# Kernel tuning notes

Measured on AMD Instinct MI355X. Metric: run time of the kernel, lower is better.

Reference implementation:

```python
import jax, jax.numpy as jnp
import numpy as np

DIM = 3            # point feature dim (xyz)
POS_HID = 64       # pos_mlp hidden
ATTN_HID = DIM * 4 # attn_mlp hidden (mult=4)
N_NBR = 16         # points per group
GROUPS = 512       # groups per batch element
MLP_D = N_NBR * DIM  # 48


def setup_inputs() -> dict:
    key = jax.random.key(0)
    ks = jax.random.split(key, 20)
    B = 32
    s = lambda *sh: 1.0 / np.sqrt(sh[0])
    inp = {
        "original_points": jax.random.normal(ks[0], (B, GROUPS, DIM), jnp.float32),
        "data": jax.random.normal(ks[1], (B, GROUPS, N_NBR, DIM), jnp.float32),
        # PointTransformerLayer params
        "w_qkv": jax.random.normal(ks[2], (DIM, DIM * 3), jnp.float32) * s(DIM),
        "pos_w1": jax.random.normal(ks[3], (3, POS_HID), jnp.float32) * s(3),
        "pos_b1": jnp.zeros((POS_HID,), jnp.float32),
        "pos_w2": jax.random.normal(ks[4], (POS_HID, DIM), jnp.float32) * s(POS_HID),
        "pos_b2": jnp.zeros((DIM,), jnp.float32),
        "attn_w1": jax.random.normal(ks[5], (DIM, ATTN_HID), jnp.float32) * s(DIM),
        "attn_b1": jnp.zeros((ATTN_HID,), jnp.float32),
        "attn_w2": jax.random.normal(ks[6], (ATTN_HID, DIM), jnp.float32) * s(ATTN_HID),
        "attn_b2": jnp.zeros((DIM,), jnp.float32),
        # downstream MLP params
        "mlp_w1": jax.random.normal(ks[7], (MLP_D, MLP_D), jnp.float32) * s(MLP_D),
        "mlp_b1": jnp.zeros((MLP_D,), jnp.float32),
        "mlp_w2": jax.random.normal(ks[8], (MLP_D, MLP_D), jnp.float32) * s(MLP_D),
        "mlp_b2": jnp.zeros((MLP_D,), jnp.float32),
        "mlp_w3": jax.random.normal(ks[9], (MLP_D, 1), jnp.float32) * s(MLP_D),
        "mlp_b3": jnp.zeros((1,), jnp.float32),
    }
    return inp


def reference(original_points, data, w_qkv, pos_w1, pos_b1, pos_w2, pos_b2,
              attn_w1, attn_b1, attn_w2, attn_b2,
              mlp_w1, mlp_b1, mlp_w2, mlp_b2, mlp_w3, mlp_b3):
    B, G, n, d = data.shape
    x = data.reshape(B * G, n, d)          # (BG, n, 3)
    pos = x[:, :, :3]                       # pos == features here (f=3)

    # Point-transformer vector attention
    qkv = x @ w_qkv                          # (BG, n, 9)
    q, k, v = jnp.split(qkv, 3, axis=-1)
    rel_pos = pos[:, :, None, :] - pos[:, None, :, :]              # (BG, n, n, 3)
    rel_emb = jax.nn.relu(rel_pos @ pos_w1 + pos_b1) @ pos_w2 + pos_b2  # (BG, n, n, 3)
    qk_rel = q[:, :, None, :] - k[:, None, :, :]                   # (BG, n, n, 3)
    v_ij = v[:, None, :, :] + rel_emb                              # (BG, n, n, 3)
    sim = jax.nn.relu((qk_rel + rel_emb) @ attn_w1 + attn_b1) @ attn_w2 + attn_b2
    attn = jax.nn.softmax(sim, axis=-2)                            # softmax over j
    agg = jnp.einsum('bijd,bijd->bid', attn, v_ij)                 # (BG, n, 3)

    # regroup into (B, 512, 48) exactly as stack(split(512, dim=0))
    sa = agg.reshape(B, G, n * d)
    h = jax.nn.relu(sa @ mlp_w1 + mlp_b1)
    h = jax.nn.relu(h @ mlp_w2 + mlp_b2)
    return h @ mlp_w3 + mlp_b3              # (B, 512, 1)
```

## Files before the change

kernel.cpp:

```cpp
#include <hip/hip_runtime.h>


typedef _Float16 h2 __attribute__((ext_vector_type(2)));
typedef _Float16 h8 __attribute__((ext_vector_type(8)));

#define AH_STRIDE 36

union H8U { h8 v; h2 p[4]; unsigned u[4]; };

__device__ __forceinline__ h2 pkrtz(float a, float b) {
    return __builtin_bit_cast(h2, __builtin_amdgcn_cvt_pkrtz(a, b));
}
__device__ __forceinline__ h2 uash2(unsigned u) {
    return __builtin_bit_cast(h2, u);
}

#if __has_builtin(__builtin_amdgcn_fdot2)
__device__ __forceinline__ float dot2acc(h2 a, h2 b, float c) {
    return __builtin_amdgcn_fdot2(a, b, c, false);
}
#else
__device__ __forceinline__ float dot2acc(h2 a, h2 b, float c) {
    return fmaf((float)a.x, (float)b.x, fmaf((float)a.y, (float)b.y, c));
}
#endif

__device__ __forceinline__ float dpp_add16(float x) {
    float s = x;
    int t;
    t = __builtin_amdgcn_update_dpp(0, __builtin_bit_cast(int, s), 0x121, 0xf, 0xf, false);
    s += __builtin_bit_cast(float, t);
    t = __builtin_amdgcn_update_dpp(0, __builtin_bit_cast(int, s), 0x122, 0xf, 0xf, false);
    s += __builtin_bit_cast(float, t);
    t = __builtin_amdgcn_update_dpp(0, __builtin_bit_cast(int, s), 0x124, 0xf, 0xf, false);
    s += __builtin_bit_cast(float, t);
    t = __builtin_amdgcn_update_dpp(0, __builtin_bit_cast(int, s), 0x128, 0xf, 0xf, false);
    s += __builtin_bit_cast(float, t);
    return s;
}

__global__ void wpack(const float* __restrict__ pw2, const float* __restrict__ aw1,
                      const float* __restrict__ ab1, const float* __restrict__ aw2,
                      unsigned* __restrict__ ws) {
    const int t = threadIdx.x;
    if (t < 96) {
        const int hp = t & 31, c = t >> 5;
        ws[c*32+hp] = __builtin_bit_cast(unsigned, pkrtz(pw2[(2*hp)*3+c], pw2[(2*hp+1)*3+c]));
    } else if (t < 114) {
        const int idx = t - 96, r = idx / 6, gp = idx % 6;
        ws[96+r*6+gp] = __builtin_bit_cast(unsigned, pkrtz(aw1[r*12+2*gp], aw1[r*12+2*gp+1]));
    } else if (t < 120) {
        const int gp = t - 114;
        ws[114+gp] = __builtin_bit_cast(unsigned, pkrtz(ab1[2*gp], ab1[2*gp+1]));
    } else if (t < 138) {
        const int idx = t - 120, gp = idx / 3, c = idx % 3;
        ws[120+gp*3+c] = __builtin_bit_cast(unsigned, pkrtz(aw2[(2*gp)*3+c], aw2[(2*gp+1)*3+c]));
    }
}

__global__ __launch_bounds__(256) void pt_main(
    const float* __restrict__ data,
    const float* __restrict__ wqkv,
    const float* __restrict__ pw1,
    const float* __restrict__ pb1,
    const float* __restrict__ pb2,
    const float* __restrict__ ab2,
    const float* __restrict__ mw1,
    const float* __restrict__ mb1,
    const float* __restrict__ mw2,
    const float* __restrict__ mb2,
    const float* __restrict__ mw3,
    const float* __restrict__ mb3,
    const unsigned* __restrict__ wsp,
    float* __restrict__ out)
{
    __shared__ __attribute__((aligned(16))) float s_pos[48];
    __shared__ __attribute__((aligned(16))) float s_q4[64], s_k4[64], s_v4[64];
    __shared__ __attribute__((aligned(16))) float s_sa[48], s_h1[48];
    __shared__ __attribute__((aligned(16))) unsigned s_a1h[16 * AH_STRIDE];
    __shared__ __attribute__((aligned(16))) unsigned s_a2h[16 * AH_STRIDE];

    const int g = blockIdx.x;
    const int t = threadIdx.x;

    if (t < 48) s_pos[t] = data[g * 48 + t];
    __syncthreads();

    if (t < 48) {
        const int sec = t >> 4, p = t & 15;
        const float x0 = s_pos[p*3+0], x1 = s_pos[p*3+1], x2 = s_pos[p*3+2];
        float* dst = (sec == 0) ? s_q4 : (sec == 1) ? s_k4 : s_v4;
        #pragma unroll
        for (int c = 0; c < 3; ++c) {
            dst[p*4+c] = fmaf(x0, wqkv[0*9 + sec*3 + c],
                         fmaf(x1, wqkv[1*9 + sec*3 + c],
                         x2 * wqkv[2*9 + sec*3 + c]));
        }
        dst[p*4+3] = 0.0f;
    }

    {
        const int ii = t >> 4;
        const int hc = (t & 15) << 2;
        const float x0 = s_pos[ii*3+0], x1 = s_pos[ii*3+1], x2 = s_pos[ii*3+2];
        float s[4];
        #pragma unroll
        for (int c = 0; c < 4; ++c) {
            const int h = hc + c;
            s[c] = fmaf(x0, pw1[h], fmaf(x1, pw1[64+h], x2 * pw1[128+h]));
        }
        h2 a1p0 = pkrtz(s[0] + pb1[hc+0], s[1] + pb1[hc+1]);
        h2 a1p1 = pkrtz(s[2] + pb1[hc+2], s[3] + pb1[hc+3]);
        h2 a2p0 = pkrtz(s[0], s[1]);
        h2 a2p1 = pkrtz(s[2], s[3]);
        const int base = ii * AH_STRIDE + (hc >> 1);
        s_a1h[base+0] = __builtin_bit_cast(unsigned, a1p0);
        s_a1h[base+1] = __builtin_bit_cast(unsigned, a1p1);
        s_a2h[base+0] = __builtin_bit_cast(unsigned, a2p0);
        s_a2h[base+1] = __builtin_bit_cast(unsigned, a2p1);
    }
    __syncthreads();

    const int i = t >> 4, j = t & 15;

    float e0 = pb2[0], e1 = pb2[1], e2 = pb2[2];
    #pragma unroll
    for (int cc = 0; cc < 8; ++cc) {
        H8U ai, aj;
        ai.v = *(const h8*)&s_a1h[i * AH_STRIDE + cc*4];
        aj.v = *(const h8*)&s_a2h[j * AH_STRIDE + cc*4];
        #pragma unroll
        for (int m = 0; m < 4; ++m) {
            const int hp = cc*4 + m;
            h2 d = ai.p[m] - aj.p[m];
            h2 z = {(_Float16)0, (_Float16)0};
            h2 r = { d.x > z.x ? d.x : z.x, d.y > z.y ? d.y : z.y };
            e0 = dot2acc(r, uash2(wsp[0*32+hp]), e0);
            e1 = dot2acc(r, uash2(wsp[1*32+hp]), e1);
            e2 = dot2acc(r, uash2(wsp[2*32+hp]), e2);
        }
    }

    const float4 qv = *(const float4*)&s_q4[i*4];
    const float4 kv = *(const float4*)&s_k4[j*4];
    const float4 vv = *(const float4*)&s_v4[j*4];
    const float vi0 = vv.x + e0, vi1 = vv.y + e1, vi2 = vv.z + e2;
    const float si0 = qv.x - kv.x + e0;
    const float si1 = qv.y - kv.y + e1;
    const float si2 = qv.z - kv.z + e2;

    const h2 sx = pkrtz(si0, si0), sy = pkrtz(si1, si1), sz = pkrtz(si2, si2);
    const h2 z2 = {(_Float16)0, (_Float16)0};
    float m0 = ab2[0], m1 = ab2[1], m2 = ab2[2];
    #pragma unroll
    for (int gp = 0; gp < 6; ++gp) {
        h2 acc = uash2(wsp[114+gp]);
        acc = __builtin_elementwise_fma(sx, uash2(wsp[96+0*6+gp]), acc);
        acc = __builtin_elementwise_fma(sy, uash2(wsp[96+1*6+gp]), acc);
        acc = __builtin_elementwise_fma(sz, uash2(wsp[96+2*6+gp]), acc);
        h2 hg = { acc.x > z2.x ? acc.x : z2.x, acc.y > z2.y ? acc.y : z2.y };
        m0 = dot2acc(hg, uash2(wsp[120+gp*3+0]), m0);
        m1 = dot2acc(hg, uash2(wsp[120+gp*3+1]), m1);
        m2 = dot2acc(hg, uash2(wsp[120+gp*3+2]), m2);
    }

    const float L2E = 1.44269504f;
    const float p0 = __builtin_amdgcn_exp2f(m0 * L2E);
    const float p1 = __builtin_amdgcn_exp2f(m1 * L2E);
    const float p2 = __builtin_amdgcn_exp2f(m2 * L2E);

    const float n0 = dpp_add16(p0 * vi0);
    const float n1 = dpp_add16(p1 * vi1);
    const float n2 = dpp_add16(p2 * vi2);
    const float d0 = dpp_add16(p0);
    const float d1 = dpp_add16(p1);
    const float d2 = dpp_add16(p2);

    if (j == 0) {
        s_sa[i*3+0] = n0 * __builtin_amdgcn_rcpf(d0);
        s_sa[i*3+1] = n1 * __builtin_amdgcn_rcpf(d1);
        s_sa[i*3+2] = n2 * __builtin_amdgcn_rcpf(d2);
    }
    __syncthreads();

    if (t < 48) {
        float h1 = mb1[t];
        #pragma unroll
        for (int c = 0; c < 48; ++c) h1 = fmaf(s_sa[c], mw1[c*48+t], h1);
        s_h1[t] = fmaxf(h1, 0.0f);
    }
    __syncthreads();

    float fv = 0.0f;
    if (t < 48) {
        float h2v = mb2[t];
        #pragma unroll
        for (int c = 0; c < 48; ++c) h2v = fmaf(s_h1[c], mw2[c*48+t], h2v);
        h2v = fmaxf(h2v, 0.0f);
        fv = h2v * mw3[t];
    }
    if (t < 64) {
        #pragma unroll
        for (int mk = 1; mk < 64; mk <<= 1) fv += __shfl_xor(fv, mk);
        if (t == 0) out[g] = fv + mb3[0];
    }
}

extern "C" void kernel_launch(void* const* d_in, const int* in_sizes, int n_in,
                              void* d_out, int out_size, void* d_ws, size_t ws_size,
                              hipStream_t stream) {
    const float* data = (const float*)d_in[1];
    unsigned* ws = (unsigned*)d_ws;
    const int groups = out_size;

    wpack<<<1, 256, 0, stream>>>(
        (const float*)d_in[5],
        (const float*)d_in[7],
        (const float*)d_in[8],
        (const float*)d_in[9],
        ws);

    pt_main<<<groups, 256, 0, stream>>>(
        data,
        (const float*)d_in[2],
        (const float*)d_in[3],
        (const float*)d_in[4],
        (const float*)d_in[6],
        (const float*)d_in[10],
        (const float*)d_in[11],
        (const float*)d_in[12],
        (const float*)d_in[13],
        (const float*)d_in[14],
        (const float*)d_in[15],
        (const float*)d_in[16],
        ws,
        (float*)d_out);
}
```

Before: 139.3 us.

## Split tail MLP matvecs across all four waves with shared partial sums

The two 48x48 MLP layers, which ran serially in a single wave with 48-deep FMA chains, now split the input dimension across four waves. Each wave computes 12-term partial sums and writes them to shared memory, and a reduction step combines them. The final 64-lane shuffle reduction is replaced by a DPP 16-lane reduction plus readlanes, and the ReLU selects become packed elementwise max. This shortens the serial tail latency of each block at the cost of two extra barriers and more shared memory.

```diff
diff --git a/kernel.cpp b/kernel.cpp
--- a/kernel.cpp
+++ b/kernel.cpp
@@ -13,6 +13,9 @@
 }
 __device__ __forceinline__ h2 uash2(unsigned u) {
     return __builtin_bit_cast(h2, u);
+}
+__device__ __forceinline__ h2 hmax2(h2 a, h2 b) {
+    return __builtin_elementwise_max(a, b);
 }
 
 #if __has_builtin(__builtin_amdgcn_fdot2)
@@ -77,11 +80,14 @@
     __shared__ __attribute__((aligned(16))) float s_pos[48];
     __shared__ __attribute__((aligned(16))) float s_q4[64], s_k4[64], s_v4[64];
     __shared__ __attribute__((aligned(16))) float s_sa[48], s_h1[48];
+    __shared__ __attribute__((aligned(16))) float s_p[4 * 48];
     __shared__ __attribute__((aligned(16))) unsigned s_a1h[16 * AH_STRIDE];
     __shared__ __attribute__((aligned(16))) unsigned s_a2h[16 * AH_STRIDE];
 
     const int g = blockIdx.x;
     const int t = threadIdx.x;
+    const int wv = t >> 6;
+    const int o  = t & 63;
 
     if (t < 48) s_pos[t] = data[g * 48 + t];
     __syncthreads();
@@ -134,7 +140,7 @@
             const int hp = cc*4 + m;
             h2 d = ai.p[m] - aj.p[m];
             h2 z = {(_Float16)0, (_Float16)0};
-            h2 r = { d.x > z.x ? d.x : z.x, d.y > z.y ? d.y : z.y };
+            h2 r = hmax2(d, z);
             e0 = dot2acc(r, uash2(wsp[0*32+hp]), e0);
             e1 = dot2acc(r, uash2(wsp[1*32+hp]), e1);
             e2 = dot2acc(r, uash2(wsp[2*32+hp]), e2);
@@ -158,7 +164,7 @@
         acc = __builtin_elementwise_fma(sx, uash2(wsp[96+0*6+gp]), acc);
         acc = __builtin_elementwise_fma(sy, uash2(wsp[96+1*6+gp]), acc);
         acc = __builtin_elementwise_fma(sz, uash2(wsp[96+2*6+gp]), acc);
-        h2 hg = { acc.x > z2.x ? acc.x : z2.x, acc.y > z2.y ? acc.y : z2.y };
+        h2 hg = hmax2(acc, z2);
         m0 = dot2acc(hg, uash2(wsp[120+gp*3+0]), m0);
         m1 = dot2acc(hg, uash2(wsp[120+gp*3+1]), m1);
         m2 = dot2acc(hg, uash2(wsp[120+gp*3+2]), m2);
@@ -183,26 +189,58 @@
     }
     __syncthreads();
 
+    if (o < 48) {
+        const int c0 = wv * 12;
+        const float4 sa0 = *(const float4*)&s_sa[c0];
+        const float4 sa1 = *(const float4*)&s_sa[c0 + 4];
+        const float4 sa2 = *(const float4*)&s_sa[c0 + 8];
+        float pa = 0.f, pb = 0.f;
+        #pragma unroll
+        for (int c = 0; c < 4; ++c) {
+            pa = fmaf((&sa0.x)[c], mw1[(c0+c)*48+o], pa);
+            pb = fmaf((&sa1.x)[c], mw1[(c0+4+c)*48+o], pb);
+            pa = fmaf((&sa2.x)[c], mw1[(c0+8+c)*48+o], pa);
+        }
+        s_p[wv*48+o] = pa + pb;
+    }
+    __syncthreads();
+
     if (t < 48) {
-        float h1 = mb1[t];
-        #pragma unroll
-        for (int c = 0; c < 48; ++c) h1 = fmaf(s_sa[c], mw1[c*48+t], h1);
+        const float h1 = s_p[0*48+t] + s_p[1*48+t] + s_p[2*48+t] + s_p[3*48+t] + mb1[t];
         s_h1[t] = fmaxf(h1, 0.0f);
     }
     __syncthreads();
 
-    float fv = 0.0f;
-    if (t < 48) {
-        float h2v = mb2[t];
-        #pragma unroll
-        for (int c = 0; c < 48; ++c) h2v = fmaf(s_h1[c], mw2[c*48+t], h2v);
-        h2v = fmaxf(h2v, 0.0f);
-        fv = h2v * mw3[t];
-    }
+    if (o < 48) {
+        const int c0 = wv * 12;
+        const float4 hh0 = *(const float4*)&s_h1[c0];
+        const float4 hh1 = *(const float4*)&s_h1[c0 + 4];
+        const float4 hh2 = *(const float4*)&s_h1[c0 + 8];
+        float pa = 0.f, pb = 0.f;
+        #pragma unroll
+        for (int c = 0; c < 4; ++c) {
+            pa = fmaf((&hh0.x)[c], mw2[(c0+c)*48+o], pa);
+            pb = fmaf((&hh1.x)[c], mw2[(c0+4+c)*48+o], pb);
+            pa = fmaf((&hh2.x)[c], mw2[(c0+8+c)*48+o], pa);
+        }
+        s_p[wv*48+o] = pa + pb;
+    }
+    __syncthreads();
+
     if (t < 64) {
-        #pragma unroll
-        for (int mk = 1; mk < 64; mk <<= 1) fv += __shfl_xor(fv, mk);
-        if (t == 0) out[g] = fv + mb3[0];
+        float fv = 0.0f;
+        if (t < 48) {
+            const float h2v = fmaxf(
+                s_p[0*48+t] + s_p[1*48+t] + s_p[2*48+t] + s_p[3*48+t] + mb2[t], 0.0f);
+            fv = h2v * mw3[t];
+        }
+        const float r = dpp_add16(fv);
+        const int ri = __builtin_bit_cast(int, r);
+        const float tot =
+            __builtin_bit_cast(float, __builtin_amdgcn_readlane(ri, 0)) +
+            __builtin_bit_cast(float, __builtin_amdgcn_readlane(ri, 16)) +
+            __builtin_bit_cast(float, __builtin_amdgcn_readlane(ri, 32));
+        if (t == 0) out[g] = tot + mb3[0];
     }
 }
 
```

New measurement: 141.4 us. Within noise of the previous version (+1.5%).

## Pack two groups per block with two query rows per thread

Applied to the files above, without the earlier changes.

Each 256-thread block now handles two point groups, 128 threads each. Every thread computes two query rows (i and i+8) against one neighbour j, so the shared weight and neighbour loads are reused. The first shared position staging and one block barrier are removed. The two MLP layers run inside a single wave, separated by a wave barrier and using split accumulators. The final sum uses DPP and readlane instead of shuffles. This cuts the block count and per-group sync overhead, at the cost of more registers per thread and an odd-groups edge case when the group count is not even.

```diff
diff --git a/kernel.cpp b/kernel.cpp
--- a/kernel.cpp
+++ b/kernel.cpp
@@ -13,6 +13,9 @@
 }
 __device__ __forceinline__ h2 uash2(unsigned u) {
     return __builtin_bit_cast(h2, u);
+}
+__device__ __forceinline__ h2 hmax2(h2 a, h2 b) {
+    return __builtin_elementwise_max(a, b);
 }
 
 #if __has_builtin(__builtin_amdgcn_fdot2)
@@ -74,22 +77,23 @@
     const unsigned* __restrict__ wsp,
     float* __restrict__ out)
 {
-    __shared__ __attribute__((aligned(16))) float s_pos[48];
-    __shared__ __attribute__((aligned(16))) float s_q4[64], s_k4[64], s_v4[64];
-    __shared__ __attribute__((aligned(16))) float s_sa[48], s_h1[48];
-    __shared__ __attribute__((aligned(16))) unsigned s_a1h[16 * AH_STRIDE];
-    __shared__ __attribute__((aligned(16))) unsigned s_a2h[16 * AH_STRIDE];
-
-    const int g = blockIdx.x;
-    const int t = threadIdx.x;
-
-    if (t < 48) s_pos[t] = data[g * 48 + t];
-    __syncthreads();
-
-    if (t < 48) {
-        const int sec = t >> 4, p = t & 15;
-        const float x0 = s_pos[p*3+0], x1 = s_pos[p*3+1], x2 = s_pos[p*3+2];
-        float* dst = (sec == 0) ? s_q4 : (sec == 1) ? s_k4 : s_v4;
+    __shared__ __attribute__((aligned(16))) float s_q4[2][64], s_k4[2][64], s_v4[2][64];
+    __shared__ __attribute__((aligned(16))) float s_sa[2][48];
+    __shared__ __attribute__((aligned(16))) float s_h1[2][48];
+    __shared__ __attribute__((aligned(16))) unsigned s_a1h[2][16 * AH_STRIDE];
+    __shared__ __attribute__((aligned(16))) unsigned s_a2h[2][16 * AH_STRIDE];
+
+    const int t   = threadIdx.x;
+    const int grp = t >> 7;
+    const int lt  = t & 127;
+    const int g   = blockIdx.x * 2 + grp;
+
+    if (lt < 48) {
+        const int sec = lt >> 4, p = lt & 15;
+        const float x0 = data[g*48 + p*3 + 0];
+        const float x1 = data[g*48 + p*3 + 1];
+        const float x2 = data[g*48 + p*3 + 2];
+        float* dst = (sec == 0) ? s_q4[grp] : (sec == 1) ? s_k4[grp] : s_v4[grp];
         #pragma unroll
         for (int c = 0; c < 3; ++c) {
             dst[p*4+c] = fmaf(x0, wqkv[0*9 + sec*3 + c],
@@ -100,109 +104,166 @@
     }
 
     {
-        const int ii = t >> 4;
-        const int hc = (t & 15) << 2;
-        const float x0 = s_pos[ii*3+0], x1 = s_pos[ii*3+1], x2 = s_pos[ii*3+2];
-        float s[4];
+        const int p  = lt >> 3;
+        const int hc = (lt & 7) << 3;
+        const float x0 = data[g*48 + p*3 + 0];
+        const float x1 = data[g*48 + p*3 + 1];
+        const float x2 = data[g*48 + p*3 + 2];
+        const float4 w0a = *(const float4*)&pw1[hc],     w0b = *(const float4*)&pw1[hc+4];
+        const float4 w1a = *(const float4*)&pw1[64+hc],  w1b = *(const float4*)&pw1[64+hc+4];
+        const float4 w2a = *(const float4*)&pw1[128+hc], w2b = *(const float4*)&pw1[128+hc+4];
+        const float4 ba  = *(const float4*)&pb1[hc],     bb  = *(const float4*)&pb1[hc+4];
+        float s[8];
         #pragma unroll
         for (int c = 0; c < 4; ++c) {
-            const int h = hc + c;
-            s[c] = fmaf(x0, pw1[h], fmaf(x1, pw1[64+h], x2 * pw1[128+h]));
-        }
-        h2 a1p0 = pkrtz(s[0] + pb1[hc+0], s[1] + pb1[hc+1]);
-        h2 a1p1 = pkrtz(s[2] + pb1[hc+2], s[3] + pb1[hc+3]);
-        h2 a2p0 = pkrtz(s[0], s[1]);
-        h2 a2p1 = pkrtz(s[2], s[3]);
-        const int base = ii * AH_STRIDE + (hc >> 1);
-        s_a1h[base+0] = __builtin_bit_cast(unsigned, a1p0);
-        s_a1h[base+1] = __builtin_bit_cast(unsigned, a1p1);
-        s_a2h[base+0] = __builtin_bit_cast(unsigned, a2p0);
-        s_a2h[base+1] = __builtin_bit_cast(unsigned, a2p1);
+            s[c]   = fmaf(x0, (&w0a.x)[c], fmaf(x1, (&w1a.x)[c], x2 * (&w2a.x)[c]));
+            s[4+c] = fmaf(x0, (&w0b.x)[c], fmaf(x1, (&w1b.x)[c], x2 * (&w2b.x)[c]));
+        }
+        uint4 a1u, a2u;
+        a1u.x = __builtin_bit_cast(unsigned, pkrtz(s[0]+ba.x, s[1]+ba.y));
+        a1u.y = __builtin_bit_cast(unsigned, pkrtz(s[2]+ba.z, s[3]+ba.w));
+        a1u.z = __builtin_bit_cast(unsigned, pkrtz(s[4]+bb.x, s[5]+bb.y));
+        a1u.w = __builtin_bit_cast(unsigned, pkrtz(s[6]+bb.z, s[7]+bb.w));
+        a2u.x = __builtin_bit_cast(unsigned, pkrtz(s[0], s[1]));
+        a2u.y = __builtin_bit_cast(unsigned, pkrtz(s[2], s[3]));
+        a2u.z = __builtin_bit_cast(unsigned, pkrtz(s[4], s[5]));
+        a2u.w = __builtin_bit_cast(unsigned, pkrtz(s[6], s[7]));
+        const int base = p * AH_STRIDE + (hc >> 1);
+        *(uint4*)&s_a1h[grp][base] = a1u;
+        *(uint4*)&s_a2h[grp][base] = a2u;
     }
     __syncthreads();
 
-    const int i = t >> 4, j = t & 15;
-
-    float e0 = pb2[0], e1 = pb2[1], e2 = pb2[2];
+    const int i = lt >> 4, j = lt & 15, i2 = i + 8;
+
+    float eA0 = pb2[0], eA1 = pb2[1], eA2 = pb2[2];
+    float eB0 = pb2[0], eB1 = pb2[1], eB2 = pb2[2];
     #pragma unroll
     for (int cc = 0; cc < 8; ++cc) {
-        H8U ai, aj;
-        ai.v = *(const h8*)&s_a1h[i * AH_STRIDE + cc*4];
-        aj.v = *(const h8*)&s_a2h[j * AH_STRIDE + cc*4];
+        H8U aiA, aiB, aj;
+        aiA.v = *(const h8*)&s_a1h[grp][i  * AH_STRIDE + cc*4];
+        aiB.v = *(const h8*)&s_a1h[grp][i2 * AH_STRIDE + cc*4];
+        aj.v  = *(const h8*)&s_a2h[grp][j  * AH_STRIDE + cc*4];
         #pragma unroll
         for (int m = 0; m < 4; ++m) {
             const int hp = cc*4 + m;
-            h2 d = ai.p[m] - aj.p[m];
-            h2 z = {(_Float16)0, (_Float16)0};
-            h2 r = { d.x > z.x ? d.x : z.x, d.y > z.y ? d.y : z.y };
-            e0 = dot2acc(r, uash2(wsp[0*32+hp]), e0);
-            e1 = dot2acc(r, uash2(wsp[1*32+hp]), e1);
-            e2 = dot2acc(r, uash2(wsp[2*32+hp]), e2);
-        }
-    }
-
-    const float4 qv = *(const float4*)&s_q4[i*4];
-    const float4 kv = *(const float4*)&s_k4[j*4];
-    const float4 vv = *(const float4*)&s_v4[j*4];
-    const float vi0 = vv.x + e0, vi1 = vv.y + e1, vi2 = vv.z + e2;
-    const float si0 = qv.x - kv.x + e0;
-    const float si1 = qv.y - kv.y + e1;
-    const float si2 = qv.z - kv.z + e2;
-
-    const h2 sx = pkrtz(si0, si0), sy = pkrtz(si1, si1), sz = pkrtz(si2, si2);
+            const h2 z = {(_Float16)0, (_Float16)0};
+            const h2 w0 = uash2(wsp[0*32+hp]);
+            const h2 w1 = uash2(wsp[1*32+hp]);
+            const h2 w2 = uash2(wsp[2*32+hp]);
+            h2 rA = hmax2(aiA.p[m] - aj.p[m], z);
+            h2 rB = hmax2(aiB.p[m] - aj.p[m], z);
+            eA0 = dot2acc(rA, w0, eA0);
+            eA1 = dot2acc(rA, w1, eA1);
+            eA2 = dot2acc(rA, w2, eA2);
+            eB0 = dot2acc(rB, w0, eB0);
+            eB1 = dot2acc(rB, w1, eB1);
+            eB2 = dot2acc(rB, w2, eB2);
+        }
+    }
+
+    const float4 qA = *(const float4*)&s_q4[grp][i*4];
+    const float4 qB = *(const float4*)&s_q4[grp][i2*4];
+    const float4 kv = *(const float4*)&s_k4[grp][j*4];
+    const float4 vv = *(const float4*)&s_v4[grp][j*4];
+
+    const float viA0 = vv.x + eA0, viA1 = vv.y + eA1, viA2 = vv.z + eA2;
+    const float viB0 = vv.x + eB0, viB1 = vv.y + eB1, viB2 = vv.z + eB2;
+    const float siA0 = qA.x - kv.x + eA0, siA1 = qA.y - kv.y + eA1, siA2 = qA.z - kv.z + eA2;
+    const float siB0 = qB.x - kv.x + eB0, siB1 = qB.y - kv.y + eB1, siB2 = qB.z - kv.z + eB2;
+
     const h2 z2 = {(_Float16)0, (_Float16)0};
-    float m0 = ab2[0], m1 = ab2[1], m2 = ab2[2];
+    const h2 sAx = pkrtz(siA0, siA0), sAy = pkrtz(siA1, siA1), sAz = pkrtz(siA2, siA2);
+    const h2 sBx = pkrtz(siB0, siB0), sBy = pkrtz(siB1, siB1), sBz = pkrtz(siB2, siB2);
+    float mA0 = ab2[0], mA1 = ab2[1], mA2 = ab2[2];
+    float mB0 = ab2[0], mB1 = ab2[1], mB2 = ab2[2];
     #pragma unroll
     for (int gp = 0; gp < 6; ++gp) {
-        h2 acc = uash2(wsp[114+gp]);
-        acc = __builtin_elementwise_fma(sx, uash2(wsp[96+0*6+gp]), acc);
-        acc = __builtin_elementwise_fma(sy, uash2(wsp[96+1*6+gp]), acc);
-        acc = __builtin_elementwise_fma(sz, uash2(wsp[96+2*6+gp]), acc);
-        h2 hg = { acc.x > z2.x ? acc.x : z2.x, acc.y > z2.y ? acc.y : z2.y };
-        m0 = dot2acc(hg, uash2(wsp[120+gp*3+0]), m0);
-        m1 = dot2acc(hg, uash2(wsp[120+gp*3+1]), m1);
-        m2 = dot2acc(hg, uash2(wsp[120+gp*3+2]), m2);
+        const h2 b1p = uash2(wsp[114+gp]);
+        const h2 u0 = uash2(wsp[96+0*6+gp]);
+        const h2 u1 = uash2(wsp[96+1*6+gp]);
+        const h2 u2 = uash2(wsp[96+2*6+gp]);
+        const h2 v0 = uash2(wsp[120+gp*3+0]);
+        const h2 v1 = uash2(wsp[120+gp*3+1]);
+        const h2 v2 = uash2(wsp[120+gp*3+2]);
+        h2 accA = b1p, accB = b1p;
+        accA = __builtin_elementwise_fma(sAx, u0, accA);
+        accA = __builtin_elementwise_fma(sAy, u1, accA);
+        accA = __builtin_elementwise_fma(sAz, u2, accA);
+        accB = __builtin_elementwise_fma(sBx, u0, accB);
+        accB = __builtin_elementwise_fma(sBy, u1, accB);
+        accB = __builtin_elementwise_fma(sBz, u2, accB);
+        h2 hA = hmax2(accA, z2), hB = hmax2(accB, z2);
+        mA0 = dot2acc(hA, v0, mA0);
+        mA1 = dot2acc(hA, v1, mA1);
+        mA2 = dot2acc(hA, v2, mA2);
+        mB0 = dot2acc(hB, v0, mB0);
+        mB1 = dot2acc(hB, v1, mB1);
+        mB2 = dot2acc(hB, v2, mB2);
     }
 
     const float L2E = 1.44269504f;
-    const float p0 = __builtin_amdgcn_exp2f(m0 * L2E);
-    const float p1 = __builtin_amdgcn_exp2f(m1 * L2E);
-    const float p2 = __builtin_amdgcn_exp2f(m2 * L2E);
-
-    const float n0 = dpp_add16(p0 * vi0);
-    const float n1 = dpp_add16(p1 * vi1);
-    const float n2 = dpp_add16(p2 * vi2);
-    const float d0 = dpp_add16(p0);
-    const float d1 = dpp_add16(p1);
-    const float d2 = dpp_add16(p2);
+    const float pA0 = __builtin_amdgcn_exp2f(mA0 * L2E);
+    const float pA1 = __builtin_amdgcn_exp2f(mA1 * L2E);
+    const float pA2 = __builtin_amdgcn_exp2f(mA2 * L2E);
+    const float pB0 = __builtin_amdgcn_exp2f(mB0 * L2E);
+    const float pB1 = __builtin_amdgcn_exp2f(mB1 * L2E);
+    const float pB2 = __builtin_amdgcn_exp2f(mB2 * L2E);
+
+    const float nA0 = dpp_add16(pA0 * viA0);
+    const float nA1 = dpp_add16(pA1 * viA1);
+    const float nA2 = dpp_add16(pA2 * viA2);
+    const float dA0 = dpp_add16(pA0);
+    const float dA1 = dpp_add16(pA1);
+    const float dA2 = dpp_add16(pA2);
+    const float nB0 = dpp_add16(pB0 * viB0);
+    const float nB1 = dpp_add16(pB1 * viB1);
+    const float nB2 = dpp_add16(pB2 * viB2);
+    const float dB0 = dpp_add16(pB0);
+    const float dB1 = dpp_add16(pB1);
+    const float dB2 = dpp_add16(pB2);
 
     if (j == 0) {
-        s_sa[i*3+0] = n0 * __builtin_amdgcn_rcpf(d0);
-        s_sa[i*3+1] = n1 * __builtin_amdgcn_rcpf(d1);
-        s_sa[i*3+2] = n2 * __builtin_amdgcn_rcpf(d2);
+        s_sa[grp][i*3+0]  = nA0 * __builtin_amdgcn_rcpf(dA0);
+        s_sa[grp][i*3+1]  = nA1 * __builtin_amdgcn_rcpf(dA1);
+        s_sa[grp][i*3+2]  = nA2 * __builtin_amdgcn_rcpf(dA2);
+        s_sa[grp][i2*3+0] = nB0 * __builtin_amdgcn_rcpf(dB0);
+        s_sa[grp][i2*3+1] = nB1 * __builtin_amdgcn_rcpf(dB1);
+        s_sa[grp][i2*3+2] = nB2 * __builtin_amdgcn_rcpf(dB2);
     }
     __syncthreads();
 
-    if (t < 48) {
-        float h1 = mb1[t];
-        #pragma unroll
-        for (int c = 0; c < 48; ++c) h1 = fmaf(s_sa[c], mw1[c*48+t], h1);
-        s_h1[t] = fmaxf(h1, 0.0f);
-    }
-    __syncthreads();
-
-    float fv = 0.0f;
-    if (t < 48) {
-        float h2v = mb2[t];
-        #pragma unroll
-        for (int c = 0; c < 48; ++c) h2v = fmaf(s_h1[c], mw2[c*48+t], h2v);
-        h2v = fmaxf(h2v, 0.0f);
-        fv = h2v * mw3[t];
-    }
-    if (t < 64) {
-        #pragma unroll
-        for (int mk = 1; mk < 64; mk <<= 1) fv += __shfl_xor(fv, mk);
-        if (t == 0) out[g] = fv + mb3[0];
+    if (lt < 48) {
+        const int o = lt;
+        float a0 = 0.f, a1 = 0.f, a2 = 0.f, a3 = 0.f;
+        #pragma unroll
+        for (int c = 0; c < 48; c += 4) {
+            const float4 sa = *(const float4*)&s_sa[grp][c];
+            a0 = fmaf(sa.x, mw1[(c+0)*48+o], a0);
+            a1 = fmaf(sa.y, mw1[(c+1)*48+o], a1);
+            a2 = fmaf(sa.z, mw1[(c+2)*48+o], a2);
+            a3 = fmaf(sa.w, mw1[(c+3)*48+o], a3);
+        }
+        s_h1[grp][o] = fmaxf((a0+a1) + (a2+a3) + mb1[o], 0.0f);
+        __builtin_amdgcn_wave_barrier();
+        float b0 = 0.f, b1 = 0.f, b2 = 0.f, b3 = 0.f;
+        #pragma unroll
+        for (int c = 0; c < 48; c += 4) {
+            const float4 hh = *(const float4*)&s_h1[grp][c];
+            b0 = fmaf(hh.x, mw2[(c+0)*48+o], b0);
+            b1 = fmaf(hh.y, mw2[(c+1)*48+o], b1);
+            b2 = fmaf(hh.z, mw2[(c+2)*48+o], b2);
+            b3 = fmaf(hh.w, mw2[(c+3)*48+o], b3);
+        }
+        const float h2v = fmaxf((b0+b1) + (b2+b3) + mb2[o], 0.0f);
+        const float fv = h2v * mw3[o];
+        const float r = dpp_add16(fv);
+        const int ri = __builtin_bit_cast(int, r);
+        const float tot =
+            __builtin_bit_cast(float, __builtin_amdgcn_readlane(ri, 0)) +
+            __builtin_bit_cast(float, __builtin_amdgcn_readlane(ri, 16)) +
+            __builtin_bit_cast(float, __builtin_amdgcn_readlane(ri, 32));
+        if (o == 0) out[g] = tot + mb3[0];
     }
 }
 
@@ -220,7 +281,7 @@
         (const float*)d_in[9],
         ws);
 
-    pt_main<<<groups, 256, 0, stream>>>(
+    pt_main<<<groups / 2, 256, 0, stream>>>(
         data,
         (const float*)d_in[2],
         (const float*)d_in[3],
```

Result: no change. 136.9 us (-1.7%).
